# Kernel tuning notes

Hardware: AMD Instinct MI355X
Metric: run time of the kernel (lower is better)

The kernel has to match this reference:

```python
import jax, jax.numpy as jnp
import numpy as np

N = 100000   # nodes
E = 1000000  # edges
F_IN = 128
H = 64
L = 6
C = 10
G = 64       # graphs in batch


def setup_inputs() -> dict:
    key = jax.random.key(0)
    ks = jax.random.split(key, 12)
    x = jax.random.normal(ks[0], (N, F_IN), dtype=jnp.float32)
    edge_index = jax.random.randint(ks[1], (2, E), 0, N, dtype=jnp.int64)
    batch = jnp.sort(jax.random.randint(ks[2], (N,), 0, G, dtype=jnp.int64))
    s = lambda fan: 1.0 / np.sqrt(fan)
    return {
        "x": x,
        "edge_index": edge_index,
        "batch": batch,
        "W0": jax.random.normal(ks[3], (F_IN, H), dtype=jnp.float32) * s(F_IN),
        "b0": jnp.zeros((H,), jnp.float32),
        "Wh": jax.random.normal(ks[4], (L - 1, H, H), dtype=jnp.float32) * s(H),
        "bh": jnp.zeros((L - 1, H), jnp.float32),
        "jkW": jax.random.normal(ks[5], (H * L, H), dtype=jnp.float32) * s(H * L),
        "jkb": jnp.zeros((H,), jnp.float32),
        "W1": jax.random.normal(ks[6], (H, H), dtype=jnp.float32) * s(H),
        "b1": jnp.zeros((H,), jnp.float32),
        "W2": jax.random.normal(ks[7], (H, C), dtype=jnp.float32) * s(H),
        "b2": jnp.zeros((C,), jnp.float32),
    }


def reference(x, edge_index, batch, W0, b0, Wh, bh, jkW, jkb, W1, b1, W2, b2):
    n = x.shape[0]
    # add self-loops (PyG GCNConv default)
    loops = jnp.arange(n, dtype=edge_index.dtype)
    src = jnp.concatenate([edge_index[0], loops])
    dst = jnp.concatenate([edge_index[1], loops])
    # symmetric degree normalization D^{-1/2} (A+I) D^{-1/2}
    deg = jax.ops.segment_sum(jnp.ones_like(dst, x.dtype), dst, num_segments=n)
    disq = jnp.where(deg > 0, deg ** -0.5, 0.0)
    norm = (disq[src] * disq[dst])[:, None]  # [E+N, 1]

    def gcn(h, W, b):
        hW = h @ W                              # [N, H] transform first
        msg = hW[src] * norm                    # gather + normalize
        agg = jax.ops.segment_sum(msg, dst, num_segments=n)  # scatter-add
        return agg + b

    h = jax.nn.relu(gcn(x, W0, b0))
    xs = [h]
    for i in range(L - 1):
        h = jax.nn.relu(gcn(h, Wh[i], bh[i]))
        xs.append(h)
    hcat = jnp.concatenate(xs, axis=-1)         # JK 'cat' -> [N, H*L]
    h = jax.nn.relu(hcat @ jkW + jkb)
    pooled = jax.ops.segment_sum(h, batch, num_segments=G)  # global_add_pool
    h = jax.nn.relu(pooled @ W1 + b1)
    return jax.nn.softmax(h @ W2 + b2, axis=-1)  # [G, C]
```

## Files before the change

kernel.cpp:

```cpp
#include <hip/hip_runtime.h>
#include <hip/hip_fp16.h>

#define NN 100000
#define NE 1000000
#define F_INF 128
#define HID 64
#define NLAY 6
#define NCLS 10
#define NGRAPH 64
#define PART_SZ 12500

__device__ __forceinline__ float4 h4f(ushort4 u) {
    __half2 lo = *reinterpret_cast<__half2*>(&u);
    __half2 hi = *reinterpret_cast<__half2*>(reinterpret_cast<unsigned short*>(&u) + 2);
    float2 a = __half22float2(lo);
    float2 b = __half22float2(hi);
    return make_float4(a.x, a.y, b.x, b.y);
}

__device__ __forceinline__ ushort4 f4h(float4 v) {
    __half2 lo = __floats2half2_rn(v.x, v.y);
    __half2 hi = __floats2half2_rn(v.z, v.w);
    ushort4 u;
    *reinterpret_cast<__half2*>(&u) = lo;
    *reinterpret_cast<__half2*>(reinterpret_cast<unsigned short*>(&u) + 2) = hi;
    return u;
}

__global__ void k_hist(const int* __restrict__ dst, int* __restrict__ counts, int e) {
    int i = blockIdx.x * 256 + threadIdx.x;
    if (i < e) atomicAdd(&counts[dst[i]], 1);
}

__global__ void k_blocksum(const int* __restrict__ counts, int* __restrict__ bsum, int n) {
    int i = blockIdx.x * 256 + threadIdx.x;
    int v = (i < n) ? counts[i] : 0;
    #pragma unroll
    for (int off = 32; off >= 1; off >>= 1) v += __shfl_down(v, off);
    __shared__ int ws[4];
    if ((threadIdx.x & 63) == 0) ws[threadIdx.x >> 6] = v;
    __syncthreads();
    if (threadIdx.x == 0) bsum[blockIdx.x] = ws[0] + ws[1] + ws[2] + ws[3];
}

__global__ void k_scanbsum(int* __restrict__ bsum, int nb) {
    __shared__ int sh[512];
    int t = threadIdx.x;
    int v = (t < nb) ? bsum[t] : 0;
    sh[t] = v; __syncthreads();
    for (int off = 1; off < 512; off <<= 1) {
        int x = (t >= off) ? sh[t - off] : 0;
        __syncthreads();
        sh[t] += x; __syncthreads();
    }
    if (t < nb) bsum[t] = sh[t] - v;
}

__global__ void k_scanwrite(const int* __restrict__ counts, const int* __restrict__ bsumx,
                            int* __restrict__ rowptr, int* __restrict__ wptr,
                            float* __restrict__ disq, int n, int e) {
    __shared__ int sh[256];
    int t = threadIdx.x;
    int i = blockIdx.x * 256 + t;
    int v = (i < n) ? counts[i] : 0;
    sh[t] = v; __syncthreads();
    for (int off = 1; off < 256; off <<= 1) {
        int x = (t >= off) ? sh[t - off] : 0;
        __syncthreads();
        sh[t] += x; __syncthreads();
    }
    int excl = sh[t] - v + bsumx[blockIdx.x];
    if (i < n) {
        rowptr[i] = excl;
        wptr[i]   = excl;
        disq[i]   = rsqrtf((float)(v + 1));
    }
    if (i == 0) rowptr[n] = e;
}

__global__ void k_scatter_part(const int* __restrict__ src, const int* __restrict__ dst,
                               int* __restrict__ wptr, int* __restrict__ csr, int e) {
    int part = blockIdx.x & 7;
    int i = (blockIdx.x >> 3) * 256 + threadIdx.x;
    if (i < e) {
        int d = dst[i];
        if (d / PART_SZ == part) {
            int pos = atomicAdd(&wptr[d], 1);
            csr[pos] = src[i];
        }
    }
}

__global__ __launch_bounds__(256) void k_gemm_dual(
    const void* __restrict__ Araw, int lda, int K,
    const float* __restrict__ W,
    const float* __restrict__ jkw,
    const float* __restrict__ disq,
    unsigned short* __restrict__ C16,
    float* __restrict__ jkacc,
    int jk_mode, int a16, int n)
{
    __shared__ float Ws[64 * 64];
    __shared__ float Ws2[64 * 64];
    __shared__ float As[64 * 68];
    const int tid  = threadIdx.x;
    const int col4 = (tid & 15) * 4;
    const int rowq = tid >> 4;
    const int base = blockIdx.x * 64;

    {
        #pragma unroll
        for (int i = 0; i < 4; i++) {
            float4 v = *(const float4*)(W + (size_t)(i * 256 + tid) * 4);
            *(float4*)(Ws + (size_t)(i * 256 + tid) * 4) = v;
        }
        if (jk_mode) {
            #pragma unroll
            for (int i = 0; i < 4; i++) {
                float4 v = *(const float4*)(jkw + (size_t)(i * 256 + tid) * 4);
                *(float4*)(Ws2 + (size_t)(i * 256 + tid) * 4) = v;
            }
        }
        if (a16) {
            const ushort4* Ah = (const ushort4*)Araw;
            #pragma unroll
            for (int rr = 0; rr < 4; rr++) {
                int row = base + rowq + rr * 16;
                float4 v = make_float4(0.f, 0.f, 0.f, 0.f);
                if (row < n) v = h4f(Ah[(size_t)row * 16 + (tid & 15)]);
                *(float4*)(As + (size_t)(rowq + rr * 16) * 68 + col4) = v;
            }
        } else {
            const float* Af = (const float*)Araw;
            #pragma unroll
            for (int rr = 0; rr < 4; rr++) {
                int row = base + rowq + rr * 16;
                float4 v = make_float4(0.f, 0.f, 0.f, 0.f);
                if (row < n) v = *(const float4*)(Af + (size_t)row * lda + col4);
                *(float4*)(As + (size_t)(rowq + rr * 16) * 68 + col4) = v;
            }
        }
    }
    __syncthreads();

    float4 acc[4], acc2[4];
    #pragma unroll
    for (int r = 0; r < 4; r++) {
        acc[r]  = make_float4(0.f, 0.f, 0.f, 0.f);
        acc2[r] = make_float4(0.f, 0.f, 0.f, 0.f);
    }

    for (int k0 = 0; k0 < K; k0 += 64) {
        const bool more = (k0 + 64) < K;
        float4 wreg[4], areg[4];
        if (more) {
            const float* Af = (const float*)Araw;
            #pragma unroll
            for (int i = 0; i < 4; i++)
                wreg[i] = *(const float4*)(W + (size_t)(k0 + 64) * 64 + (i * 256 + tid) * 4);
            #pragma unroll
            for (int rr = 0; rr < 4; rr++) {
                int row = base + rowq + rr * 16;
                areg[rr] = make_float4(0.f, 0.f, 0.f, 0.f);
                if (row < n) areg[rr] = *(const float4*)(Af + (size_t)row * lda + k0 + 64 + col4);
            }
        }
        if (jk_mode && k0 == 0) {
            #pragma unroll 4
            for (int k = 0; k < 64; k++) {
                float4 w  = *(const float4*)(Ws  + k * 64 + col4);
                float4 w2 = *(const float4*)(Ws2 + k * 64 + col4);
                float a0 = As[(rowq * 4 + 0) * 68 + k];
                float a1 = As[(rowq * 4 + 1) * 68 + k];
                float a2 = As[(rowq * 4 + 2) * 68 + k];
                float a3 = As[(rowq * 4 + 3) * 68 + k];
                acc[0].x = fmaf(a0, w.x, acc[0].x); acc[0].y = fmaf(a0, w.y, acc[0].y);
                acc[0].z = fmaf(a0, w.z, acc[0].z); acc[0].w = fmaf(a0, w.w, acc[0].w);
                acc[1].x = fmaf(a1, w.x, acc[1].x); acc[1].y = fmaf(a1, w.y, acc[1].y);
                acc[1].z = fmaf(a1, w.z, acc[1].z); acc[1].w = fmaf(a1, w.w, acc[1].w);
                acc[2].x = fmaf(a2, w.x, acc[2].x); acc[2].y = fmaf(a2, w.y, acc[2].y);
                acc[2].z = fmaf(a2, w.z, acc[2].z); acc[2].w = fmaf(a2, w.w, acc[2].w);
                acc[3].x = fmaf(a3, w.x, acc[3].x); acc[3].y = fmaf(a3, w.y, acc[3].y);
                acc[3].z = fmaf(a3, w.z, acc[3].z); acc[3].w = fmaf(a3, w.w, acc[3].w);
                acc2[0].x = fmaf(a0, w2.x, acc2[0].x); acc2[0].y = fmaf(a0, w2.y, acc2[0].y);
                acc2[0].z = fmaf(a0, w2.z, acc2[0].z); acc2[0].w = fmaf(a0, w2.w, acc2[0].w);
                acc2[1].x = fmaf(a1, w2.x, acc2[1].x); acc2[1].y = fmaf(a1, w2.y, acc2[1].y);
                acc2[1].z = fmaf(a1, w2.z, acc2[1].z); acc2[1].w = fmaf(a1, w2.w, acc2[1].w);
                acc2[2].x = fmaf(a2, w2.x, acc2[2].x); acc2[2].y = fmaf(a2, w2.y, acc2[2].y);
                acc2[2].z = fmaf(a2, w2.z, acc2[2].z); acc2[2].w = fmaf(a2, w2.w, acc2[2].w);
                acc2[3].x = fmaf(a3, w2.x, acc2[3].x); acc2[3].y = fmaf(a3, w2.y, acc2[3].y);
                acc2[3].z = fmaf(a3, w2.z, acc2[3].z); acc2[3].w = fmaf(a3, w2.w, acc2[3].w);
            }
        } else {
            #pragma unroll 8
            for (int k = 0; k < 64; k++) {
                float4 w = *(const float4*)(Ws + k * 64 + col4);
                float a0 = As[(rowq * 4 + 0) * 68 + k];
                float a1 = As[(rowq * 4 + 1) * 68 + k];
                float a2 = As[(rowq * 4 + 2) * 68 + k];
                float a3 = As[(rowq * 4 + 3) * 68 + k];
                acc[0].x = fmaf(a0, w.x, acc[0].x); acc[0].y = fmaf(a0, w.y, acc[0].y);
                acc[0].z = fmaf(a0, w.z, acc[0].z); acc[0].w = fmaf(a0, w.w, acc[0].w);
                acc[1].x = fmaf(a1, w.x, acc[1].x); acc[1].y = fmaf(a1, w.y, acc[1].y);
                acc[1].z = fmaf(a1, w.z, acc[1].z); acc[1].w = fmaf(a1, w.w, acc[1].w);
                acc[2].x = fmaf(a2, w.x, acc[2].x); acc[2].y = fmaf(a2, w.y, acc[2].y);
                acc[2].z = fmaf(a2, w.z, acc[2].z); acc[2].w = fmaf(a2, w.w, acc[2].w);
                acc[3].x = fmaf(a3, w.x, acc[3].x); acc[3].y = fmaf(a3, w.y, acc[3].y);
                acc[3].z = fmaf(a3, w.z, acc[3].z); acc[3].w = fmaf(a3, w.w, acc[3].w);
            }
        }
        __syncthreads();
        if (more) {
            #pragma unroll
            for (int i = 0; i < 4; i++)
                *(float4*)(Ws + (size_t)(i * 256 + tid) * 4) = wreg[i];
            #pragma unroll
            for (int rr = 0; rr < 4; rr++)
                *(float4*)(As + (size_t)(rowq + rr * 16) * 68 + col4) = areg[rr];
            __syncthreads();
        }
    }

    #pragma unroll
    for (int r = 0; r < 4; r++) {
        int row = base + rowq * 4 + r;
        if (row < n) {
            float s = disq[row];
            float4 o;
            o.x = acc[r].x * s; o.y = acc[r].y * s;
            o.z = acc[r].z * s; o.w = acc[r].w * s;
            ((ushort4*)C16)[(size_t)row * 16 + (tid & 15)] = f4h(o);
            if (jk_mode == 1) {
                *(float4*)(jkacc + (size_t)row * 64 + col4) = acc2[r];
            } else if (jk_mode == 2) {
                float4 p = *(const float4*)(jkacc + (size_t)row * 64 + col4);
                p.x += acc2[r].x; p.y += acc2[r].y;
                p.z += acc2[r].z; p.w += acc2[r].w;
                *(float4*)(jkacc + (size_t)row * 64 + col4) = p;
            }
        }
    }
}

__global__ __launch_bounds__(256) void k_gather(
    const int* __restrict__ rowptr, const int* __restrict__ csr,
    const unsigned short* __restrict__ hW16, const float* __restrict__ disq,
    const float* __restrict__ bias, unsigned short* __restrict__ hout16, int n)
{
    const ushort4* hW4 = (const ushort4*)hW16;
    int wid  = (blockIdx.x * 256 + threadIdx.x) >> 6;
    if (wid >= n) return;
    int lane = threadIdx.x & 63;
    int fb = lane & 15;
    int es = lane >> 4;
    int j  = rowptr[wid];
    int r1 = rowptr[wid + 1];
    float4 v  = make_float4(0.f, 0.f, 0.f, 0.f);
    float4 v2 = make_float4(0.f, 0.f, 0.f, 0.f);
    if (es == 0) v = h4f(hW4[(size_t)wid * 16 + fb]);
    while (j < r1) {
        int cnt = min(r1 - j, 64);
        int idx = (lane < cnt) ? csr[j + lane] : 0;
        for (int jj = 0; jj < cnt; jj += 16) {
            int i0 = jj + es, i1 = jj + 4 + es, i2 = jj + 8 + es, i3 = jj + 12 + es;
            int s0 = __shfl(idx, i0 & 63);
            int s1 = __shfl(idx, i1 & 63);
            int s2 = __shfl(idx, i2 & 63);
            int s3 = __shfl(idx, i3 & 63);
            float4 t0 = h4f(hW4[(size_t)s0 * 16 + fb]);
            float4 t1 = h4f(hW4[(size_t)s1 * 16 + fb]);
            float4 t2 = h4f(hW4[(size_t)s2 * 16 + fb]);
            float4 t3 = h4f(hW4[(size_t)s3 * 16 + fb]);
            if (i0 < cnt) { v.x  += t0.x; v.y  += t0.y; v.z  += t0.z; v.w  += t0.w; }
            if (i1 < cnt) { v2.x += t1.x; v2.y += t1.y; v2.z += t1.z; v2.w += t1.w; }
            if (i2 < cnt) { v.x  += t2.x; v.y  += t2.y; v.z  += t2.z; v.w  += t2.w; }
            if (i3 < cnt) { v2.x += t3.x; v2.y += t3.y; v2.z += t3.z; v2.w += t3.w; }
        }
        j += cnt;
    }
    v.x += v2.x; v.y += v2.y; v.z += v2.z; v.w += v2.w;
    v.x += __shfl_xor(v.x, 16); v.y += __shfl_xor(v.y, 16);
    v.z += __shfl_xor(v.z, 16); v.w += __shfl_xor(v.w, 16);
    v.x += __shfl_xor(v.x, 32); v.y += __shfl_xor(v.y, 32);
    v.z += __shfl_xor(v.z, 32); v.w += __shfl_xor(v.w, 32);
    if (es == 0) {
        float s = disq[wid];
        float4 b = ((const float4*)bias)[fb];
        float4 o;
        o.x = fmaxf(fmaf(s, v.x, b.x), 0.f);
        o.y = fmaxf(fmaf(s, v.y, b.y), 0.f);
        o.z = fmaxf(fmaf(s, v.z, b.z), 0.f);
        o.w = fmaxf(fmaf(s, v.w, b.w), 0.f);
        ((ushort4*)hout16)[(size_t)wid * 16 + fb] = f4h(o);
    }
}

__global__ __launch_bounds__(256) void k_jkfin_pool(
    const unsigned short* __restrict__ A16,
    const float* __restrict__ W,
    const float* __restrict__ jkacc,
    const float* __restrict__ bias,
    const int* __restrict__ batch,
    float* __restrict__ pooled,
    int n)
{
    __shared__ float Ws[64 * 64];
    __shared__ float As[64 * 68];
    const int tid  = threadIdx.x;
    const int col4 = (tid & 15) * 4;
    const int rowq = tid >> 4;
    const int base = blockIdx.x * 64;

    #pragma unroll
    for (int i = 0; i < 4; i++) {
        float4 v = *(const float4*)(W + (size_t)(i * 256 + tid) * 4);
        *(float4*)(Ws + (size_t)(i * 256 + tid) * 4) = v;
    }
    {
        const ushort4* Ah = (const ushort4*)A16;
        #pragma unroll
        for (int rr = 0; rr < 4; rr++) {
            int row = base + rowq + rr * 16;
            float4 v = make_float4(0.f, 0.f, 0.f, 0.f);
            if (row < n) v = h4f(Ah[(size_t)row * 16 + (tid & 15)]);
            *(float4*)(As + (size_t)(rowq + rr * 16) * 68 + col4) = v;
        }
    }
    __syncthreads();

    float4 acc[4];
    #pragma unroll
    for (int r = 0; r < 4; r++) acc[r] = make_float4(0.f, 0.f, 0.f, 0.f);
    #pragma unroll 8
    for (int k = 0; k < 64; k++) {
        float4 w = *(const float4*)(Ws + k * 64 + col4);
        float a0 = As[(rowq * 4 + 0) * 68 + k];
        float a1 = As[(rowq * 4 + 1) * 68 + k];
        float a2 = As[(rowq * 4 + 2) * 68 + k];
        float a3 = As[(rowq * 4 + 3) * 68 + k];
        acc[0].x = fmaf(a0, w.x, acc[0].x); acc[0].y = fmaf(a0, w.y, acc[0].y);
        acc[0].z = fmaf(a0, w.z, acc[0].z); acc[0].w = fmaf(a0, w.w, acc[0].w);
        acc[1].x = fmaf(a1, w.x, acc[1].x); acc[1].y = fmaf(a1, w.y, acc[1].y);
        acc[1].z = fmaf(a1, w.z, acc[1].z); acc[1].w = fmaf(a1, w.w, acc[1].w);
        acc[2].x = fmaf(a2, w.x, acc[2].x); acc[2].y = fmaf(a2, w.y, acc[2].y);
        acc[2].z = fmaf(a2, w.z, acc[2].z); acc[2].w = fmaf(a2, w.w, acc[2].w);
        acc[3].x = fmaf(a3, w.x, acc[3].x); acc[3].y = fmaf(a3, w.y, acc[3].y);
        acc[3].z = fmaf(a3, w.z, acc[3].z); acc[3].w = fmaf(a3, w.w, acc[3].w);
    }
    __syncthreads();

    float* slab = Ws;
    #pragma unroll
    for (int i = tid; i < 4096; i += 256) slab[i] = 0.f;
    __syncthreads();

    float4 bb = *(const float4*)(bias + col4);
    int curg = -1;
    float4 s4 = make_float4(0.f, 0.f, 0.f, 0.f);
    #pragma unroll
    for (int r = 0; r < 4; r++) {
        int row = base + rowq * 4 + r;
        if (row < n) {
            float4 p = *(const float4*)(jkacc + (size_t)row * 64 + col4);
            float4 vv;
            vv.x = fmaxf(acc[r].x + p.x + bb.x, 0.f);
            vv.y = fmaxf(acc[r].y + p.y + bb.y, 0.f);
            vv.z = fmaxf(acc[r].z + p.z + bb.z, 0.f);
            vv.w = fmaxf(acc[r].w + p.w + bb.w, 0.f);
            int g = batch[row];
            if (g != curg) {
                if (curg >= 0) {
                    atomicAdd(&slab[curg * 64 + col4 + 0], s4.x);
                    atomicAdd(&slab[curg * 64 + col4 + 1], s4.y);
                    atomicAdd(&slab[curg * 64 + col4 + 2], s4.z);
                    atomicAdd(&slab[curg * 64 + col4 + 3], s4.w);
                }
                curg = g; s4 = vv;
            } else {
                s4.x += vv.x; s4.y += vv.y; s4.z += vv.z; s4.w += vv.w;
            }
        }
    }
    if (curg >= 0) {
        atomicAdd(&slab[curg * 64 + col4 + 0], s4.x);
        atomicAdd(&slab[curg * 64 + col4 + 1], s4.y);
        atomicAdd(&slab[curg * 64 + col4 + 2], s4.z);
        atomicAdd(&slab[curg * 64 + col4 + 3], s4.w);
    }
    __syncthreads();

    int g0 = batch[base];
    int g1 = batch[(base + 63 < n) ? (base + 63) : (n - 1)];
    int cnt = (g1 - g0 + 1) * 64;
    for (int i = tid; i < cnt; i += 256) {
        int g = g0 + (i >> 6);
        int c = i & 63;
        float v = slab[g * 64 + c];
        if (v != 0.f) atomicAdd(&pooled[g * 64 + c], v);
    }
}

__global__ __launch_bounds__(64) void k_head(
    const float* __restrict__ pooled,
    const float* __restrict__ W1, const float* __restrict__ b1,
    const float* __restrict__ W2, const float* __restrict__ b2,
    float* __restrict__ out)
{
    __shared__ float p[64];
    __shared__ float h1[64];
    __shared__ float lg[16];
    const int g = blockIdx.x;
    const int t = threadIdx.x;

    p[t] = pooled[g * 64 + t];
    __syncthreads();

    float acc = b1[t];
    #pragma unroll 8
    for (int k = 0; k < 64; k++) acc = fmaf(p[k], W1[k * 64 + t], acc);
    h1[t] = fmaxf(acc, 0.f);
    __syncthreads();

    if (t < NCLS) {
        float a = b2[t];
        #pragma unroll 8
        for (int j = 0; j < 64; j++) a = fmaf(h1[j], W2[j * NCLS + t], a);
        lg[t] = a;
    }
    __syncthreads();

    if (t == 0) {
        float mx = lg[0];
        #pragma unroll
        for (int c = 1; c < NCLS; c++) mx = fmaxf(mx, lg[c]);
        float ssum = 0.f;
        float e[NCLS];
        #pragma unroll
        for (int c = 0; c < NCLS; c++) { e[c] = __expf(lg[c] - mx); ssum += e[c]; }
        float inv = 1.0f / ssum;
        #pragma unroll
        for (int c = 0; c < NCLS; c++) out[g * NCLS + c] = e[c] * inv;
    }
}

extern "C" void kernel_launch(void* const* d_in, const int* in_sizes, int n_in,
                              void* d_out, int out_size, void* d_ws, size_t ws_size,
                              hipStream_t stream) {
    (void)in_sizes; (void)n_in; (void)out_size; (void)ws_size;
    const float* x     = (const float*)d_in[0];
    const int*   ei    = (const int*)d_in[1];
    const int*   batch = (const int*)d_in[2];
    const float* W0    = (const float*)d_in[3];
    const float* b0    = (const float*)d_in[4];
    const float* Wh    = (const float*)d_in[5];
    const float* bh    = (const float*)d_in[6];
    const float* jkW   = (const float*)d_in[7];
    const float* jkb   = (const float*)d_in[8];
    const float* W1    = (const float*)d_in[9];
    const float* b1    = (const float*)d_in[10];
    const float* W2    = (const float*)d_in[11];
    const float* b2    = (const float*)d_in[12];

    const int* src = ei;
    const int* dst = ei + NE;

    float*          fws    = (float*)d_ws;
    float*          disq   = fws;
    unsigned short* hWb    = (unsigned short*)(disq + 100352);
    unsigned short* h16    = hWb + (size_t)NN * 64;
    float*          jkacc  = (float*)(h16 + (size_t)NN * 64);
    float*          pooled = jkacc + (size_t)NN * 64;
    int*            counts = (int*)(pooled + 4096);
    int*            rowptr = counts + 100352;
    int*            wptr   = rowptr + 100352;
    int*            bsum   = wptr + 100352;
    int*            csr    = bsum + 512;

    const int NB_N = (NN + 255) / 256;
    const int NB_E = (NE + 255) / 256;

    hipMemsetAsync(counts, 0, (size_t)NN * sizeof(int), stream);
    k_hist<<<NB_E, 256, 0, stream>>>(dst, counts, NE);
    k_blocksum<<<NB_N, 256, 0, stream>>>(counts, bsum, NN);
    k_scanbsum<<<1, 512, 0, stream>>>(bsum, NB_N);
    k_scanwrite<<<NB_N, 256, 0, stream>>>(counts, bsum, rowptr, wptr, disq, NN, NE);
    k_scatter_part<<<NB_E * 8, 256, 0, stream>>>(src, dst, wptr, csr, NE);

    const int gemm_grid   = (NN + 63) / 64;
    const int gather_grid = (NN + 3) / 4;
    for (int l = 0; l < NLAY; l++) {
        const void*  A    = (l == 0) ? (const void*)x : (const void*)h16;
        int          a16  = (l == 0) ? 0 : 1;
        int          lda  = (l == 0) ? F_INF : HID;
        int          K    = (l == 0) ? F_INF : HID;
        const float* W    = (l == 0) ? W0 : (Wh + (size_t)(l - 1) * 64 * 64);
        const float* bias = (l == 0) ? b0 : (bh + (size_t)(l - 1) * 64);
        const float* jw   = (l == 0) ? nullptr : (jkW + (size_t)(l - 1) * 64 * 64);
        int          jkm  = (l == 0) ? 0 : ((l == 1) ? 1 : 2);

        k_gemm_dual<<<gemm_grid, 256, 0, stream>>>(A, lda, K, W, jw, disq,
                                                   hWb, jkacc, jkm, a16, NN);
        k_gather<<<gather_grid, 256, 0, stream>>>(rowptr, csr, hWb, disq, bias, h16, NN);
    }

    hipMemsetAsync(pooled, 0, 64 * 64 * sizeof(float), stream);
    k_jkfin_pool<<<gemm_grid, 256, 0, stream>>>(h16, jkW + (size_t)5 * 64 * 64, jkacc,
                                                jkb, batch, pooled, NN);
    k_head<<<NGRAPH, 64, 0, stream>>>(pooled, W1, b1, W2, b2, (float*)d_out);
}
```

Measured before the change: 550.7 us.

## Fuse CSR scatter with layer-0 GEMM and specialize hidden-layer GEMM kernel

Merges the partitioned edge scatter and the first-layer x@W0 transform into one launch, with separate block ranges doing independent work, so the two can overlap and one launch is saved. The hidden-layer GEMM becomes a dedicated fp16-input, K=64 kernel without runtime branches on jk_mode or input type. Histogram and scatter threads each process several edges to cut block count. The combined kernel's shared-memory footprint applies to the scatter blocks as well, which may limit their occupancy.

```diff
diff --git a/kernel.cpp b/kernel.cpp
--- a/kernel.cpp
+++ b/kernel.cpp
@@ -9,6 +9,8 @@
 #define NCLS 10
 #define NGRAPH 64
 #define PART_SZ 12500
+#define SCAT_BLKS (((NE + 2047) / 2048) * 8)
+#define GEMM_GRID ((NN + 63) / 64)
 
 __device__ __forceinline__ float4 h4f(ushort4 u) {
     __half2 lo = *reinterpret_cast<__half2*>(&u);
@@ -28,8 +30,12 @@
 }
 
 __global__ void k_hist(const int* __restrict__ dst, int* __restrict__ counts, int e) {
-    int i = blockIdx.x * 256 + threadIdx.x;
-    if (i < e) atomicAdd(&counts[dst[i]], 1);
+    int i0 = blockIdx.x * 1024 + threadIdx.x;
+    #pragma unroll
+    for (int k = 0; k < 4; k++) {
+        int i = i0 + k * 256;
+        if (i < e) atomicAdd(&counts[dst[i]], 1);
+    }
 }
 
 __global__ void k_blocksum(const int* __restrict__ counts, int* __restrict__ bsum, int n) {
@@ -78,136 +84,84 @@
     if (i == 0) rowptr[n] = e;
 }
 
-__global__ void k_scatter_part(const int* __restrict__ src, const int* __restrict__ dst,
-                               int* __restrict__ wptr, int* __restrict__ csr, int e) {
-    int part = blockIdx.x & 7;
-    int i = (blockIdx.x >> 3) * 256 + threadIdx.x;
-    if (i < e) {
-        int d = dst[i];
-        if (d / PART_SZ == part) {
-            int pos = atomicAdd(&wptr[d], 1);
-            csr[pos] = src[i];
-        }
-    }
-}
-
-__global__ __launch_bounds__(256) void k_gemm_dual(
-    const void* __restrict__ Araw, int lda, int K,
-    const float* __restrict__ W,
-    const float* __restrict__ jkw,
-    const float* __restrict__ disq,
-    unsigned short* __restrict__ C16,
-    float* __restrict__ jkacc,
-    int jk_mode, int a16, int n)
+__global__ __launch_bounds__(256) void k_scatter_gemm0(
+    const int* __restrict__ src, const int* __restrict__ dst,
+    int* __restrict__ wptr, int* __restrict__ csr, int e,
+    const float* __restrict__ x, const float* __restrict__ W0,
+    const float* __restrict__ disq, unsigned short* __restrict__ C16, int n)
 {
     __shared__ float Ws[64 * 64];
-    __shared__ float Ws2[64 * 64];
     __shared__ float As[64 * 68];
+
+    if (blockIdx.x < SCAT_BLKS) {
+        int part = blockIdx.x & 7;
+        int i0 = (blockIdx.x >> 3) * 2048 + threadIdx.x;
+        #pragma unroll
+        for (int k = 0; k < 8; k++) {
+            int i = i0 + k * 256;
+            if (i < e) {
+                int d = dst[i];
+                if (d / PART_SZ == part) {
+                    int pos = atomicAdd(&wptr[d], 1);
+                    csr[pos] = src[i];
+                }
+            }
+        }
+        return;
+    }
+
     const int tid  = threadIdx.x;
     const int col4 = (tid & 15) * 4;
     const int rowq = tid >> 4;
-    const int base = blockIdx.x * 64;
-
-    {
-        #pragma unroll
-        for (int i = 0; i < 4; i++) {
-            float4 v = *(const float4*)(W + (size_t)(i * 256 + tid) * 4);
-            *(float4*)(Ws + (size_t)(i * 256 + tid) * 4) = v;
-        }
-        if (jk_mode) {
-            #pragma unroll
-            for (int i = 0; i < 4; i++) {
-                float4 v = *(const float4*)(jkw + (size_t)(i * 256 + tid) * 4);
-                *(float4*)(Ws2 + (size_t)(i * 256 + tid) * 4) = v;
-            }
-        }
-        if (a16) {
-            const ushort4* Ah = (const ushort4*)Araw;
-            #pragma unroll
-            for (int rr = 0; rr < 4; rr++) {
-                int row = base + rowq + rr * 16;
-                float4 v = make_float4(0.f, 0.f, 0.f, 0.f);
-                if (row < n) v = h4f(Ah[(size_t)row * 16 + (tid & 15)]);
-                *(float4*)(As + (size_t)(rowq + rr * 16) * 68 + col4) = v;
-            }
-        } else {
-            const float* Af = (const float*)Araw;
-            #pragma unroll
-            for (int rr = 0; rr < 4; rr++) {
-                int row = base + rowq + rr * 16;
-                float4 v = make_float4(0.f, 0.f, 0.f, 0.f);
-                if (row < n) v = *(const float4*)(Af + (size_t)row * lda + col4);
-                *(float4*)(As + (size_t)(rowq + rr * 16) * 68 + col4) = v;
-            }
-        }
-    }
-    __syncthreads();
-
-    float4 acc[4], acc2[4];
-    #pragma unroll
-    for (int r = 0; r < 4; r++) {
-        acc[r]  = make_float4(0.f, 0.f, 0.f, 0.f);
-        acc2[r] = make_float4(0.f, 0.f, 0.f, 0.f);
-    }
-
-    for (int k0 = 0; k0 < K; k0 += 64) {
-        const bool more = (k0 + 64) < K;
+    const int base = (blockIdx.x - SCAT_BLKS) * 64;
+
+    #pragma unroll
+    for (int i = 0; i < 4; i++) {
+        float4 v = *(const float4*)(W0 + (size_t)(i * 256 + tid) * 4);
+        *(float4*)(Ws + (size_t)(i * 256 + tid) * 4) = v;
+    }
+    #pragma unroll
+    for (int rr = 0; rr < 4; rr++) {
+        int row = base + rowq + rr * 16;
+        float4 v = make_float4(0.f, 0.f, 0.f, 0.f);
+        if (row < n) v = *(const float4*)(x + (size_t)row * F_INF + col4);
+        *(float4*)(As + (size_t)(rowq + rr * 16) * 68 + col4) = v;
+    }
+    __syncthreads();
+
+    float4 acc[4];
+    #pragma unroll
+    for (int r = 0; r < 4; r++) acc[r] = make_float4(0.f, 0.f, 0.f, 0.f);
+
+    for (int k0 = 0; k0 < F_INF; k0 += 64) {
+        const bool more = (k0 + 64) < F_INF;
         float4 wreg[4], areg[4];
         if (more) {
-            const float* Af = (const float*)Araw;
             #pragma unroll
             for (int i = 0; i < 4; i++)
-                wreg[i] = *(const float4*)(W + (size_t)(k0 + 64) * 64 + (i * 256 + tid) * 4);
+                wreg[i] = *(const float4*)(W0 + (size_t)(k0 + 64) * 64 + (i * 256 + tid) * 4);
             #pragma unroll
             for (int rr = 0; rr < 4; rr++) {
                 int row = base + rowq + rr * 16;
                 areg[rr] = make_float4(0.f, 0.f, 0.f, 0.f);
-                if (row < n) areg[rr] = *(const float4*)(Af + (size_t)row * lda + k0 + 64 + col4);
+                if (row < n) areg[rr] = *(const float4*)(x + (size_t)row * F_INF + k0 + 64 + col4);
             }
         }
-        if (jk_mode && k0 == 0) {
-            #pragma unroll 4
-            for (int k = 0; k < 64; k++) {
-                float4 w  = *(const float4*)(Ws  + k * 64 + col4);
-                float4 w2 = *(const float4*)(Ws2 + k * 64 + col4);
-                float a0 = As[(rowq * 4 + 0) * 68 + k];
-                float a1 = As[(rowq * 4 + 1) * 68 + k];
-                float a2 = As[(rowq * 4 + 2) * 68 + k];
-                float a3 = As[(rowq * 4 + 3) * 68 + k];
-                acc[0].x = fmaf(a0, w.x, acc[0].x); acc[0].y = fmaf(a0, w.y, acc[0].y);
-                acc[0].z = fmaf(a0, w.z, acc[0].z); acc[0].w = fmaf(a0, w.w, acc[0].w);
-                acc[1].x = fmaf(a1, w.x, acc[1].x); acc[1].y = fmaf(a1, w.y, acc[1].y);
-                acc[1].z = fmaf(a1, w.z, acc[1].z); acc[1].w = fmaf(a1, w.w, acc[1].w);
-                acc[2].x = fmaf(a2, w.x, acc[2].x); acc[2].y = fmaf(a2, w.y, acc[2].y);
-                acc[2].z = fmaf(a2, w.z, acc[2].z); acc[2].w = fmaf(a2, w.w, acc[2].w);
-                acc[3].x = fmaf(a3, w.x, acc[3].x); acc[3].y = fmaf(a3, w.y, acc[3].y);
-                acc[3].z = fmaf(a3, w.z, acc[3].z); acc[3].w = fmaf(a3, w.w, acc[3].w);
-                acc2[0].x = fmaf(a0, w2.x, acc2[0].x); acc2[0].y = fmaf(a0, w2.y, acc2[0].y);
-                acc2[0].z = fmaf(a0, w2.z, acc2[0].z); acc2[0].w = fmaf(a0, w2.w, acc2[0].w);
-                acc2[1].x = fmaf(a1, w2.x, acc2[1].x); acc2[1].y = fmaf(a1, w2.y, acc2[1].y);
-                acc2[1].z = fmaf(a1, w2.z, acc2[1].z); acc2[1].w = fmaf(a1, w2.w, acc2[1].w);
-                acc2[2].x = fmaf(a2, w2.x, acc2[2].x); acc2[2].y = fmaf(a2, w2.y, acc2[2].y);
-                acc2[2].z = fmaf(a2, w2.z, acc2[2].z); acc2[2].w = fmaf(a2, w2.w, acc2[2].w);
-                acc2[3].x = fmaf(a3, w2.x, acc2[3].x); acc2[3].y = fmaf(a3, w2.y, acc2[3].y);
-                acc2[3].z = fmaf(a3, w2.z, acc2[3].z); acc2[3].w = fmaf(a3, w2.w, acc2[3].w);
-            }
-        } else {
-            #pragma unroll 8
-            for (int k = 0; k < 64; k++) {
-                float4 w = *(const float4*)(Ws + k * 64 + col4);
-                float a0 = As[(rowq * 4 + 0) * 68 + k];
-                float a1 = As[(rowq * 4 + 1) * 68 + k];
-                float a2 = As[(rowq * 4 + 2) * 68 + k];
-                float a3 = As[(rowq * 4 + 3) * 68 + k];
-                acc[0].x = fmaf(a0, w.x, acc[0].x); acc[0].y = fmaf(a0, w.y, acc[0].y);
-                acc[0].z = fmaf(a0, w.z, acc[0].z); acc[0].w = fmaf(a0, w.w, acc[0].w);
-                acc[1].x = fmaf(a1, w.x, acc[1].x); acc[1].y = fmaf(a1, w.y, acc[1].y);
-                acc[1].z = fmaf(a1, w.z, acc[1].z); acc[1].w = fmaf(a1, w.w, acc[1].w);
-                acc[2].x = fmaf(a2, w.x, acc[2].x); acc[2].y = fmaf(a2, w.y, acc[2].y);
-                acc[2].z = fmaf(a2, w.z, acc[2].z); acc[2].w = fmaf(a2, w.w, acc[2].w);
-                acc[3].x = fmaf(a3, w.x, acc[3].x); acc[3].y = fmaf(a3, w.y, acc[3].y);
-                acc[3].z = fmaf(a3, w.z, acc[3].z); acc[3].w = fmaf(a3, w.w, acc[3].w);
-            }
+        #pragma unroll 8
+        for (int k = 0; k < 64; k++) {
+            float4 w = *(const float4*)(Ws + k * 64 + col4);
+            float a0 = As[(rowq * 4 + 0) * 68 + k];
+            float a1 = As[(rowq * 4 + 1) * 68 + k];
+            float a2 = As[(rowq * 4 + 2) * 68 + k];
+            float a3 = As[(rowq * 4 + 3) * 68 + k];
+            acc[0].x = fmaf(a0, w.x, acc[0].x); acc[0].y = fmaf(a0, w.y, acc[0].y);
+            acc[0].z = fmaf(a0, w.z, acc[0].z); acc[0].w = fmaf(a0, w.w, acc[0].w);
+            acc[1].x = fmaf(a1, w.x, acc[1].x); acc[1].y = fmaf(a1, w.y, acc[1].y);
+            acc[1].z = fmaf(a1, w.z, acc[1].z); acc[1].w = fmaf(a1, w.w, acc[1].w);
+            acc[2].x = fmaf(a2, w.x, acc[2].x); acc[2].y = fmaf(a2, w.y, acc[2].y);
+            acc[2].z = fmaf(a2, w.z, acc[2].z); acc[2].w = fmaf(a2, w.w, acc[2].w);
+            acc[3].x = fmaf(a3, w.x, acc[3].x); acc[3].y = fmaf(a3, w.y, acc[3].y);
+            acc[3].z = fmaf(a3, w.z, acc[3].z); acc[3].w = fmaf(a3, w.w, acc[3].w);
         }
         __syncthreads();
         if (more) {
@@ -219,6 +173,88 @@
                 *(float4*)(As + (size_t)(rowq + rr * 16) * 68 + col4) = areg[rr];
             __syncthreads();
         }
+    }
+
+    #pragma unroll
+    for (int r = 0; r < 4; r++) {
+        int row = base + rowq * 4 + r;
+        if (row < n) {
+            float s = disq[row];
+            float4 o;
+            o.x = acc[r].x * s; o.y = acc[r].y * s;
+            o.z = acc[r].z * s; o.w = acc[r].w * s;
+            ((ushort4*)C16)[(size_t)row * 16 + (tid & 15)] = f4h(o);
+        }
+    }
+}
+
+__global__ __launch_bounds__(256) void k_gemm_dual(
+    const unsigned short* __restrict__ A16,
+    const float* __restrict__ W,
+    const float* __restrict__ jkw,
+    const float* __restrict__ disq,
+    unsigned short* __restrict__ C16,
+    float* __restrict__ jkacc,
+    int jk_mode, int n)
+{
+    __shared__ float Ws[64 * 64];
+    __shared__ float Ws2[64 * 64];
+    __shared__ float As[64 * 68];
+    const int tid  = threadIdx.x;
+    const int col4 = (tid & 15) * 4;
+    const int rowq = tid >> 4;
+    const int base = blockIdx.x * 64;
+
+    #pragma unroll
+    for (int i = 0; i < 4; i++) {
+        float4 v = *(const float4*)(W + (size_t)(i * 256 + tid) * 4);
+        *(float4*)(Ws + (size_t)(i * 256 + tid) * 4) = v;
+        float4 v2 = *(const float4*)(jkw + (size_t)(i * 256 + tid) * 4);
+        *(float4*)(Ws2 + (size_t)(i * 256 + tid) * 4) = v2;
+    }
+    {
+        const ushort4* Ah = (const ushort4*)A16;
+        #pragma unroll
+        for (int rr = 0; rr < 4; rr++) {
+            int row = base + rowq + rr * 16;
+            float4 v = make_float4(0.f, 0.f, 0.f, 0.f);
+            if (row < n) v = h4f(Ah[(size_t)row * 16 + (tid & 15)]);
+            *(float4*)(As + (size_t)(rowq + rr * 16) * 68 + col4) = v;
+        }
+    }
+    __syncthreads();
+
+    float4 acc[4], acc2[4];
+    #pragma unroll
+    for (int r = 0; r < 4; r++) {
+        acc[r]  = make_float4(0.f, 0.f, 0.f, 0.f);
+        acc2[r] = make_float4(0.f, 0.f, 0.f, 0.f);
+    }
+
+    #pragma unroll 4
+    for (int k = 0; k < 64; k++) {
+        float4 w  = *(const float4*)(Ws  + k * 64 + col4);
+        float4 w2 = *(const float4*)(Ws2 + k * 64 + col4);
+        float a0 = As[(rowq * 4 + 0) * 68 + k];
+        float a1 = As[(rowq * 4 + 1) * 68 + k];
+        float a2 = As[(rowq * 4 + 2) * 68 + k];
+        float a3 = As[(rowq * 4 + 3) * 68 + k];
+        acc[0].x = fmaf(a0, w.x, acc[0].x); acc[0].y = fmaf(a0, w.y, acc[0].y);
+        acc[0].z = fmaf(a0, w.z, acc[0].z); acc[0].w = fmaf(a0, w.w, acc[0].w);
+        acc[1].x = fmaf(a1, w.x, acc[1].x); acc[1].y = fmaf(a1, w.y, acc[1].y);
+        acc[1].z = fmaf(a1, w.z, acc[1].z); acc[1].w = fmaf(a1, w.w, acc[1].w);
+        acc[2].x = fmaf(a2, w.x, acc[2].x); acc[2].y = fmaf(a2, w.y, acc[2].y);
+        acc[2].z = fmaf(a2, w.z, acc[2].z); acc[2].w = fmaf(a2, w.w, acc[2].w);
+        acc[3].x = fmaf(a3, w.x, acc[3].x); acc[3].y = fmaf(a3, w.y, acc[3].y);
+        acc[3].z = fmaf(a3, w.z, acc[3].z); acc[3].w = fmaf(a3, w.w, acc[3].w);
+        acc2[0].x = fmaf(a0, w2.x, acc2[0].x); acc2[0].y = fmaf(a0, w2.y, acc2[0].y);
+        acc2[0].z = fmaf(a0, w2.z, acc2[0].z); acc2[0].w = fmaf(a0, w2.w, acc2[0].w);
+        acc2[1].x = fmaf(a1, w2.x, acc2[1].x); acc2[1].y = fmaf(a1, w2.y, acc2[1].y);
+        acc2[1].z = fmaf(a1, w2.z, acc2[1].z); acc2[1].w = fmaf(a1, w2.w, acc2[1].w);
+        acc2[2].x = fmaf(a2, w2.x, acc2[2].x); acc2[2].y = fmaf(a2, w2.y, acc2[2].y);
+        acc2[2].z = fmaf(a2, w2.z, acc2[2].z); acc2[2].w = fmaf(a2, w2.w, acc2[2].w);
+        acc2[3].x = fmaf(a3, w2.x, acc2[3].x); acc2[3].y = fmaf(a3, w2.y, acc2[3].y);
+        acc2[3].z = fmaf(a3, w2.z, acc2[3].z); acc2[3].w = fmaf(a3, w2.w, acc2[3].w);
     }
 
     #pragma unroll
@@ -232,7 +268,7 @@
             ((ushort4*)C16)[(size_t)row * 16 + (tid & 15)] = f4h(o);
             if (jk_mode == 1) {
                 *(float4*)(jkacc + (size_t)row * 64 + col4) = acc2[r];
-            } else if (jk_mode == 2) {
+            } else {
                 float4 p = *(const float4*)(jkacc + (size_t)row * 64 + col4);
                 p.x += acc2[r].x; p.y += acc2[r].y;
                 p.z += acc2[r].z; p.w += acc2[r].w;
@@ -477,34 +513,29 @@
     int*            csr    = bsum + 512;
 
     const int NB_N = (NN + 255) / 256;
-    const int NB_E = (NE + 255) / 256;
 
     hipMemsetAsync(counts, 0, (size_t)NN * sizeof(int), stream);
-    k_hist<<<NB_E, 256, 0, stream>>>(dst, counts, NE);
+    k_hist<<<(NE + 1023) / 1024, 256, 0, stream>>>(dst, counts, NE);
     k_blocksum<<<NB_N, 256, 0, stream>>>(counts, bsum, NN);
     k_scanbsum<<<1, 512, 0, stream>>>(bsum, NB_N);
     k_scanwrite<<<NB_N, 256, 0, stream>>>(counts, bsum, rowptr, wptr, disq, NN, NE);
-    k_scatter_part<<<NB_E * 8, 256, 0, stream>>>(src, dst, wptr, csr, NE);
-
-    const int gemm_grid   = (NN + 63) / 64;
+
+    k_scatter_gemm0<<<SCAT_BLKS + GEMM_GRID, 256, 0, stream>>>(
+        src, dst, wptr, csr, NE, x, W0, disq, hWb, NN);
+
     const int gather_grid = (NN + 3) / 4;
-    for (int l = 0; l < NLAY; l++) {
-        const void*  A    = (l == 0) ? (const void*)x : (const void*)h16;
-        int          a16  = (l == 0) ? 0 : 1;
-        int          lda  = (l == 0) ? F_INF : HID;
-        int          K    = (l == 0) ? F_INF : HID;
-        const float* W    = (l == 0) ? W0 : (Wh + (size_t)(l - 1) * 64 * 64);
-        const float* bias = (l == 0) ? b0 : (bh + (size_t)(l - 1) * 64);
-        const float* jw   = (l == 0) ? nullptr : (jkW + (size_t)(l - 1) * 64 * 64);
-        int          jkm  = (l == 0) ? 0 : ((l == 1) ? 1 : 2);
-
-        k_gemm_dual<<<gemm_grid, 256, 0, stream>>>(A, lda, K, W, jw, disq,
-                                                   hWb, jkacc, jkm, a16, NN);
-        k_gather<<<gather_grid, 256, 0, stream>>>(rowptr, csr, hWb, disq, bias, h16, NN);
+    k_gather<<<gather_grid, 256, 0, stream>>>(rowptr, csr, hWb, disq, b0, h16, NN);
+    for (int l = 1; l < NLAY; l++) {
+        const float* W   = Wh + (size_t)(l - 1) * 64 * 64;
+        const float* jw  = jkW + (size_t)(l - 1) * 64 * 64;
+        int          jkm = (l == 1) ? 1 : 2;
+        k_gemm_dual<<<GEMM_GRID, 256, 0, stream>>>(h16, W, jw, disq, hWb, jkacc, jkm, NN);
+        k_gather<<<gather_grid, 256, 0, stream>>>(rowptr, csr, hWb, disq,
+                                                  bh + (size_t)(l - 1) * 64, h16, NN);
     }
 
     hipMemsetAsync(pooled, 0, 64 * 64 * sizeof(float), stream);
-    k_jkfin_pool<<<gemm_grid, 256, 0, stream>>>(h16, jkW + (size_t)5 * 64 * 64, jkacc,
+    k_jkfin_pool<<<GEMM_GRID, 256, 0, stream>>>(h16, jkW + (size_t)5 * 64 * 64, jkacc,
                                                 jkb, batch, pooled, NN);
     k_head<<<NGRAPH, 64, 0, stream>>>(pooled, W1, b1, W2, b2, (float*)d_out);
 }
```

After: 513.7 us. -6.7%, faster.
